# Kernel optimization log

Measured on AMD Instinct MI355X. Metric: run time of the kernel, lower is better.

Reference implementation:

```python
import math
import jax, jax.numpy as jnp
import numpy as np

VOCAB = 30522
HIDDEN = 768
TYPE_VOCAB = 2
EPS = 1e-12
MAX_LEN = 5000


def sin_table(dim, max_len=MAX_LEN):
    pos = jnp.arange(max_len, dtype=jnp.float32)[:, None]
    div = jnp.exp(jnp.arange(0, dim, 2, dtype=jnp.float32) * (-(math.log(10000.0) / dim)))
    ang = pos * div  # [max_len, dim//2]
    pe = jnp.zeros((max_len, dim), dtype=jnp.float32)
    pe = pe.at[:, 0::2].set(jnp.sin(ang))
    pe = pe.at[:, 1::2].set(jnp.cos(ang))
    return pe


def setup_inputs() -> dict:
    key = jax.random.key(0)
    k1, k2, k3, k4, k5, k6, k7 = jax.random.split(key, 7)
    B, S = 8, 4096
    input_ids = jax.random.randint(k1, (B, S), 0, VOCAB, dtype=jnp.int64 if jax.config.jax_enable_x64 else jnp.int32)
    tok_struct_vec = jax.random.randint(k2, (B, S, 3), 0, S, dtype=input_ids.dtype)
    sent_struct_vec = jax.random.randint(k3, (B, 64, 2), 0, 64, dtype=input_ids.dtype)
    token_type_ids = jax.random.randint(k4, (B, S), 0, TYPE_VOCAB, dtype=input_ids.dtype)
    word_emb = jax.random.normal(k5, (VOCAB, HIDDEN), dtype=jnp.float32) * 0.02
    word_emb = word_emb.at[0].set(0.0)  # padding_idx=0
    type_emb = jax.random.normal(k6, (TYPE_VOCAB, HIDDEN), dtype=jnp.float32) * 0.02
    ln_w = jnp.ones((HIDDEN,), dtype=jnp.float32)
    ln_b = jnp.zeros((HIDDEN,), dtype=jnp.float32)
    return {"input_ids": input_ids, "tok_struct_vec": tok_struct_vec,
            "sent_struct_vec": sent_struct_vec, "token_type_ids": token_type_ids,
            "word_emb": word_emb, "type_emb": type_emb, "ln_w": ln_w, "ln_b": ln_b}


def reference(input_ids, tok_struct_vec, sent_struct_vec, token_type_ids,
              word_emb, type_emb, ln_w, ln_b):
    B, S = input_ids.shape
    pe = sin_table(HIDDEN)[:S]            # [S, H]
    hs_pe = sin_table(HIDDEN // 3)[:S]    # [S, H/3]

    words = word_emb[input_ids]           # [B,S,H]
    tt = type_emb[token_type_ids]         # [B,S,H]

    # NOTE: faithful to source bug: compute_se closes over para_pos, so all
    # three struct embeddings gather with para_pos (tok_struct_vec[:,:,0]).
    para_pos = tok_struct_vec[:, :, 0]
    g = hs_pe[para_pos]                   # [B,S,H/3]
    struct = jnp.concatenate((g, g, g), axis=2)  # [B,S,H]

    emb = words + pe[None, :, :] + tt + struct
    mu = jnp.mean(emb, axis=-1, keepdims=True)
    var = jnp.mean(jnp.square(emb - mu), axis=-1, keepdims=True)
    out = (emb - mu) / jnp.sqrt(var + EPS) * ln_w + ln_b
    return out  # dropout is identity in eval mode
```

## Files before the change

### kernel.cpp

```cpp
#include <hip/hip_runtime.h>
#include <math.h>

#define HIDDEN 768

#define K768 (-0.011992630692677323f)
#define K256 (-0.035977892078031970f)
#define C256 (0.04641588833612779f)
#define C512 (0.002154434690031884f)

__global__ __launch_bounds__(256) void emb_ln_kernel(
    const int*   __restrict__ input_ids,
    const int*   __restrict__ tok_struct,
    const int*   __restrict__ token_type,
    const float* __restrict__ word_emb,
    const float* __restrict__ type_emb,
    const float* __restrict__ ln_w,
    const float* __restrict__ ln_b,
    float*       __restrict__ out,
    int S)
{
    const int wave = threadIdx.x >> 6;
    const int lane = threadIdx.x & 63;
    const int row  = blockIdx.x * 4 + wave;
    const int s    = row & (S - 1);

    const int id   = input_ids[row];
    const int tt   = token_type[row];
    const int ppos = tok_struct[row * 3];

    const int h0 = lane * 4;

    const float d0 = __expf((float)h0 * K256);
    const float d1 = __expf((float)(h0 + 2) * K256);
    const float pp = (float)ppos;
    float hs[4];
    hs[0] = __sinf(pp * d0);
    hs[1] = __cosf(pp * d0);
    hs[2] = __sinf(pp * d1);
    hs[3] = __cosf(pp * d1);

    const float e0 = __expf((float)h0 * K768);
    const float e2 = __expf((float)(h0 + 2) * K768);
    const float fs = (float)s;

    const float4* wrow = (const float4*)(word_emb + (size_t)id * HIDDEN);
    const float4* trow = (const float4*)(type_emb + (size_t)tt * HIDDEN);

    float v[12];
#pragma unroll
    for (int j = 0; j < 3; ++j) {
        const float scale = (j == 0) ? 1.0f : (j == 1 ? C256 : C512);
        const float a0 = fs * (e0 * scale);
        const float a1 = fs * (e2 * scale);
        const float pe0 = __sinf(a0);
        const float pe1 = __cosf(a0);
        const float pe2 = __sinf(a1);
        const float pe3 = __cosf(a1);

        const float4 w  = wrow[lane + 64 * j];
        const float4 ty = trow[lane + 64 * j];

        v[4 * j + 0] = w.x + ty.x + pe0 + hs[0];
        v[4 * j + 1] = w.y + ty.y + pe1 + hs[1];
        v[4 * j + 2] = w.z + ty.z + pe2 + hs[2];
        v[4 * j + 3] = w.w + ty.w + pe3 + hs[3];
    }

    float s1 = 0.0f, s2 = 0.0f;
#pragma unroll
    for (int i = 0; i < 12; ++i) {
        s1 += v[i];
        s2 = fmaf(v[i], v[i], s2);
    }
#pragma unroll
    for (int off = 1; off < 64; off <<= 1) {
        s1 += __shfl_xor(s1, off, 64);
        s2 += __shfl_xor(s2, off, 64);
    }

    const float inv_n = 1.0f / (float)HIDDEN;
    const float mu  = s1 * inv_n;
    float var = s2 * inv_n - mu * mu;
    var = fmaxf(var, 0.0f);
    const float rstd = rsqrtf(var + 1e-12f);

    const float4* wv = (const float4*)ln_w;
    const float4* bv = (const float4*)ln_b;
    float4* orow = (float4*)(out + (size_t)row * HIDDEN);
#pragma unroll
    for (int j = 0; j < 3; ++j) {
        const float4 g = wv[lane + 64 * j];
        const float4 b = bv[lane + 64 * j];
        float4 r;
        r.x = (v[4 * j + 0] - mu) * rstd * g.x + b.x;
        r.y = (v[4 * j + 1] - mu) * rstd * g.y + b.y;
        r.z = (v[4 * j + 2] - mu) * rstd * g.z + b.z;
        r.w = (v[4 * j + 3] - mu) * rstd * g.w + b.w;
        orow[lane + 64 * j] = r;
    }
}

extern "C" void kernel_launch(void* const* d_in, const int* in_sizes, int n_in,
                              void* d_out, int out_size, void* d_ws, size_t ws_size,
                              hipStream_t stream) {
    const int*   input_ids  = (const int*)  d_in[0];
    const int*   tok_struct = (const int*)  d_in[1];
    const int*   token_type = (const int*)  d_in[3];
    const float* word_emb   = (const float*)d_in[4];
    const float* type_emb   = (const float*)d_in[5];
    const float* ln_w       = (const float*)d_in[6];
    const float* ln_b       = (const float*)d_in[7];
    float* out = (float*)d_out;

    const int BS = in_sizes[0];
    const int B  = in_sizes[2] / 128;
    const int S  = BS / B;

    emb_ln_kernel<<<BS / 4, 256, 0, stream>>>(input_ids, tok_struct, token_type,
                                              word_emb, type_emb, ln_w, ln_b,
                                              out, S);
}
```

Baseline: 191.4 us.

## Use persistent grid-stride waves with row prefetch, cached params, nontemporal stores

Launches a fixed grid of 2048 blocks in which each wave walks over rows grid-stride, prefetching the next row's ids and word-embedding vectors while computing the current row. LayerNorm weight, bias and both type-embedding rows are loaded once per wave into registers, and outputs use nontemporal stores. The goal is to hide gather latency and cut redundant parameter loads and launch overhead, at the cost of higher register pressure and lower occupancy.

```diff
diff --git a/kernel.cpp b/kernel.cpp
--- a/kernel.cpp
+++ b/kernel.cpp
@@ -8,6 +8,8 @@
 #define C256 (0.04641588833612779f)
 #define C512 (0.002154434690031884f)
 
+typedef float nfloat4 __attribute__((ext_vector_type(4)));
+
 __global__ __launch_bounds__(256) void emb_ln_kernel(
     const int*   __restrict__ input_ids,
     const int*   __restrict__ tok_struct,
@@ -17,86 +19,113 @@
     const float* __restrict__ ln_w,
     const float* __restrict__ ln_b,
     float*       __restrict__ out,
-    int S)
+    int S, int BS)
 {
     const int wave = threadIdx.x >> 6;
     const int lane = threadIdx.x & 63;
-    const int row  = blockIdx.x * 4 + wave;
-    const int s    = row & (S - 1);
-
-    const int id   = input_ids[row];
-    const int tt   = token_type[row];
-    const int ppos = tok_struct[row * 3];
+    const int gw   = blockIdx.x * 4 + wave;
+    const int NW   = gridDim.x * 4;
 
     const int h0 = lane * 4;
 
     const float d0 = __expf((float)h0 * K256);
     const float d1 = __expf((float)(h0 + 2) * K256);
-    const float pp = (float)ppos;
-    float hs[4];
-    hs[0] = __sinf(pp * d0);
-    hs[1] = __cosf(pp * d0);
-    hs[2] = __sinf(pp * d1);
-    hs[3] = __cosf(pp * d1);
-
     const float e0 = __expf((float)h0 * K768);
     const float e2 = __expf((float)(h0 + 2) * K768);
-    const float fs = (float)s;
 
-    const float4* wrow = (const float4*)(word_emb + (size_t)id * HIDDEN);
-    const float4* trow = (const float4*)(type_emb + (size_t)tt * HIDDEN);
-
-    float v[12];
+    float4 g[3], bb[3], t0[3], t1[3];
+    const float4* wv = (const float4*)ln_w;
+    const float4* bv = (const float4*)ln_b;
+    const float4* te = (const float4*)type_emb;
 #pragma unroll
     for (int j = 0; j < 3; ++j) {
-        const float scale = (j == 0) ? 1.0f : (j == 1 ? C256 : C512);
-        const float a0 = fs * (e0 * scale);
-        const float a1 = fs * (e2 * scale);
-        const float pe0 = __sinf(a0);
-        const float pe1 = __cosf(a0);
-        const float pe2 = __sinf(a1);
-        const float pe3 = __cosf(a1);
-
-        const float4 w  = wrow[lane + 64 * j];
-        const float4 ty = trow[lane + 64 * j];
-
-        v[4 * j + 0] = w.x + ty.x + pe0 + hs[0];
-        v[4 * j + 1] = w.y + ty.y + pe1 + hs[1];
-        v[4 * j + 2] = w.z + ty.z + pe2 + hs[2];
-        v[4 * j + 3] = w.w + ty.w + pe3 + hs[3];
+        g[j]  = wv[lane + 64 * j];
+        bb[j] = bv[lane + 64 * j];
+        t0[j] = te[lane + 64 * j];
+        t1[j] = te[lane + 64 * j + 192];
     }
 
-    float s1 = 0.0f, s2 = 0.0f;
+    int r = gw;
+    if (r >= BS) return;
+
+    int id = input_ids[r];
+    int tt = token_type[r];
+    int pp = tok_struct[3 * r];
+    float4 w[3];
+    {
+        const float4* wrow = (const float4*)(word_emb + (size_t)id * HIDDEN);
 #pragma unroll
-    for (int i = 0; i < 12; ++i) {
-        s1 += v[i];
-        s2 = fmaf(v[i], v[i], s2);
-    }
-#pragma unroll
-    for (int off = 1; off < 64; off <<= 1) {
-        s1 += __shfl_xor(s1, off, 64);
-        s2 += __shfl_xor(s2, off, 64);
+        for (int j = 0; j < 3; ++j) w[j] = wrow[lane + 64 * j];
     }
 
-    const float inv_n = 1.0f / (float)HIDDEN;
-    const float mu  = s1 * inv_n;
-    float var = s2 * inv_n - mu * mu;
-    var = fmaxf(var, 0.0f);
-    const float rstd = rsqrtf(var + 1e-12f);
+    while (true) {
+        const int rn = r + NW;
+        const bool has_next = rn < BS;
 
-    const float4* wv = (const float4*)ln_w;
-    const float4* bv = (const float4*)ln_b;
-    float4* orow = (float4*)(out + (size_t)row * HIDDEN);
+        int idn = 0, ttn = 0, ppn = 0;
+        float4 wn[3];
+        if (has_next) {
+            idn = input_ids[rn];
+            ttn = token_type[rn];
+            ppn = tok_struct[3 * rn];
+            const float4* wrow = (const float4*)(word_emb + (size_t)idn * HIDDEN);
 #pragma unroll
-    for (int j = 0; j < 3; ++j) {
-        const float4 g = wv[lane + 64 * j];
-        const float4 b = bv[lane + 64 * j];
-        float4 r;
-        r.x = (v[4 * j + 0] - mu) * rstd * g.x + b.x;
-        r.y = (v[4 * j + 1] - mu) * rstd * g.y + b.y;
-        r.z = (v[4 * j + 2] - mu) * rstd * g.z + b.z;
-        r.w = (v[4 * j + 3] - mu) * rstd * g.w + b.w;
-        orow[lane + 64 * j] = r;
+            for (int j = 0; j < 3; ++j) wn[j] = wrow[lane + 64 * j];
+        }
+
+        const float fpp = (float)pp;
+        float hs[4];
+        hs[0] = __sinf(fpp * d0);
+        hs[1] = __cosf(fpp * d0);
+        hs[2] = __sinf(fpp * d1);
+        hs[3] = __cosf(fpp * d1);
+
+        const float fs = (float)(r & (S - 1));
+
+        float v[12];
+#pragma unroll
+        for (int j = 0; j < 3; ++j) {
+            const float scale = (j == 0) ? 1.0f : (j == 1 ? C256 : C512);
+            const float a0 = fs * (e0 * scale);
+            const float a1 = fs * (e2 * scale);
+            const float4 ty = tt ? t1[j] : t0[j];
+            v[4 * j + 0] = w[j].x + ty.x + __sinf(a0) + hs[0];
+            v[4 * j + 1] = w[j].y + ty.y + __cosf(a0) + hs[1];
+            v[4 * j + 2] = w[j].z + ty.z + __sinf(a1) + hs[2];
+            v[4 * j + 3] = w[j].w + ty.w + __cosf(a1) + hs[3];
+        }
+
+        float s1 = 0.0f, s2 = 0.0f;
+#pragma unroll
+        for (int i = 0; i < 12; ++i) {
+            s1 += v[i];
+            s2 = fmaf(v[i], v[i], s2);
+        }
+#pragma unroll
+        for (int off = 1; off < 64; off <<= 1) {
+            s1 += __shfl_xor(s1, off, 64);
+            s2 += __shfl_xor(s2, off, 64);
+        }
+
+        const float inv_n = 1.0f / (float)HIDDEN;
+        const float mu = s1 * inv_n;
+        const float rstd = rsqrtf(fmaxf(s2 * inv_n - mu * mu, 0.0f) + 1e-12f);
+
+        nfloat4* orow = (nfloat4*)(out + (size_t)r * HIDDEN);
+#pragma unroll
+        for (int j = 0; j < 3; ++j) {
+            nfloat4 rr;
+            rr.x = (v[4 * j + 0] - mu) * rstd * g[j].x + bb[j].x;
+            rr.y = (v[4 * j + 1] - mu) * rstd * g[j].y + bb[j].y;
+            rr.z = (v[4 * j + 2] - mu) * rstd * g[j].z + bb[j].z;
+            rr.w = (v[4 * j + 3] - mu) * rstd * g[j].w + bb[j].w;
+            __builtin_nontemporal_store(rr, &orow[lane + 64 * j]);
+        }
+
+        if (!has_next) break;
+        id = idn; tt = ttn; pp = ppn;
+        w[0] = wn[0]; w[1] = wn[1]; w[2] = wn[2];
+        r = rn;
     }
 }
 
@@ -116,7 +145,9 @@
     const int B  = in_sizes[2] / 128;
     const int S  = BS / B;
 
-    emb_ln_kernel<<<BS / 4, 256, 0, stream>>>(input_ids, tok_struct, token_type,
+    int blocks = 2048;
+    if (blocks * 4 > BS) blocks = (BS + 3) / 4;
+    emb_ln_kernel<<<blocks, 256, 0, stream>>>(input_ids, tok_struct, token_type,
                                               word_emb, type_emb, ln_w, ln_b,
-                                              out, S);
+                                              out, S, BS);
 }
```

Result: no change. 188.7 us (-1.4%).
